# Performance work log

Hardware: AMD Instinct MI355X
Metric: run time of the kernel (lower is better)

Reference implementation:

```python
import jax, jax.numpy as jnp
import numpy as np

D_IN = 1024
D_OUT = 1024
N_HEADS = 16
HEAD_DIM = D_IN // N_HEADS      # 64
HEAD_DIM_V = D_OUT // N_HEADS   # 64


def setup_inputs() -> dict:
    key = jax.random.key(0)
    ks = jax.random.split(key, 7)
    s = 0.02
    x = jax.random.normal(ks[0], (4, 2048, D_IN), dtype=jnp.float32)
    Wq = jax.random.normal(ks[1], (D_IN, D_IN), dtype=jnp.float32) * s
    bq = jnp.zeros((D_IN,), dtype=jnp.float32)
    Wk = jax.random.normal(ks[2], (D_IN, D_IN), dtype=jnp.float32) * s
    bk = jnp.zeros((D_IN,), dtype=jnp.float32)
    Wv = jax.random.normal(ks[3], (D_IN, D_OUT), dtype=jnp.float32) * s
    bv = jnp.zeros((D_OUT,), dtype=jnp.float32)
    return {"x": x, "Wq": Wq, "bq": bq, "Wk": Wk, "bk": bk, "Wv": Wv, "bv": bv}


def reference(x, Wq, bq, Wk, bk, Wv, bv):
    B, S, _ = x.shape
    scale = jnp.sqrt(jnp.asarray(HEAD_DIM, dtype=jnp.float32))
    # projections -> [B, S, H, Dh] -> [B, H, S, Dh]
    q = (x @ Wq + bq).reshape(B, S, N_HEADS, HEAD_DIM).transpose(0, 2, 1, 3)
    k = (x @ Wk + bk).reshape(B, S, N_HEADS, HEAD_DIM).transpose(0, 2, 1, 3)
    v = (x @ Wv + bv).reshape(B, S, N_HEADS, HEAD_DIM_V).transpose(0, 2, 1, 3)
    # [B, H, S, S] attention scores (naive full materialization, as in source)
    scores = jnp.einsum("bhsd,bhtd->bhst", q, k) / scale
    weights = jax.nn.softmax(scores, axis=-1)
    out = jnp.einsum("bhst,bhtd->bhsd", weights, v)
    # [B, H, S, Dv] -> [B, S, H*Dv]  (out_projection NOT applied in source forward)
    return out.transpose(0, 2, 1, 3).reshape(B, S, N_HEADS * HEAD_DIM_V)
```

## Files before the change

### kernel.cpp

```cpp
#include <hip/hip_runtime.h>

#define B_  4
#define S_  2048
#define D_  1024
#define H_  16
#define DH_ 64
#define M_  (B_ * S_)

typedef __attribute__((ext_vector_type(8))) short short8;
typedef __attribute__((ext_vector_type(4))) float floatx4;

__device__ __forceinline__ float bf2f(unsigned short u) {
    union { unsigned int i; float f; } v; v.i = ((unsigned int)u) << 16; return v.f;
}
__device__ __forceinline__ unsigned short f2bf(float f) {
    union { float f; unsigned int i; } v; v.f = f;
    unsigned int r = v.i + 0x7fffu + ((v.i >> 16) & 1u);
    return (unsigned short)(r >> 16);
}
__device__ __forceinline__ unsigned int pk_trunc(float a, float b) {
#if __has_builtin(__builtin_amdgcn_perm)
    return __builtin_amdgcn_perm(__float_as_uint(b), __float_as_uint(a), 0x07060302u);
#else
    return (__float_as_uint(a) >> 16) | (__float_as_uint(b) & 0xffff0000u);
#endif
}

#if __has_builtin(__builtin_amdgcn_exp2f)
#define EXP2(x) __builtin_amdgcn_exp2f(x)
#else
#define EXP2(x) __expf(0.6931471805599453f * (x))
#endif

typedef const __attribute__((address_space(1))) unsigned int* gas_ptr;
typedef __attribute__((address_space(3))) unsigned int* las_ptr;
__device__ __forceinline__ void async_cp16(const void* g, void* l) {
    __builtin_amdgcn_global_load_lds((gas_ptr)g, (las_ptr)l, 16, 0, 0);
}

#define VMC4 asm volatile("s_waitcnt vmcnt(4)" ::: "memory")
#define VMC0 asm volatile("s_waitcnt vmcnt(0)" ::: "memory")

__global__ __launch_bounds__(256) void cast_x_kernel(
    const float* __restrict__ x, unsigned short* __restrict__ Ax)
{
    int i4 = blockIdx.x * 256 + threadIdx.x;
    float4 v = reinterpret_cast<const float4*>(x)[i4];
    ushort4 o;
    o.x = f2bf(v.x); o.y = f2bf(v.y); o.z = f2bf(v.z); o.w = f2bf(v.w);
    reinterpret_cast<ushort4*>(Ax)[i4] = o;
}

__global__ __launch_bounds__(256) void cast_w_T_kernel(
    const float* __restrict__ W0, const float* __restrict__ W1,
    const float* __restrict__ W2,
    unsigned short* __restrict__ T0, unsigned short* __restrict__ T1,
    unsigned short* __restrict__ T2)
{
    const float* W = blockIdx.z == 0 ? W0 : (blockIdx.z == 1 ? W1 : W2);
    unsigned short* Wt = blockIdx.z == 0 ? T0 : (blockIdx.z == 1 ? T1 : T2);

    __shared__ unsigned short T[64][72];
    const int t = threadIdx.x;
    const int k0 = blockIdx.x * 64, n0 = blockIdx.y * 64;

    #pragma unroll
    for (int p = 0; p < 4; ++p) {
        int kr = p * 16 + (t >> 4);
        int nc = (t & 15) * 4;
        float4 v = *reinterpret_cast<const float4*>(W + (size_t)(k0 + kr) * D_ + n0 + nc);
        T[nc + 0][kr] = f2bf(v.x);
        T[nc + 1][kr] = f2bf(v.y);
        T[nc + 2][kr] = f2bf(v.z);
        T[nc + 3][kr] = f2bf(v.w);
    }
    __syncthreads();

    const int nl = t >> 2, kc = (t & 3) * 16;
    size_t base = (size_t)(n0 + nl) * D_ + k0 + kc;
    *reinterpret_cast<short8*>(Wt + base)     = *reinterpret_cast<const short8*>(&T[nl][kc]);
    *reinterpret_cast<short8*>(Wt + base + 8) = *reinterpret_cast<const short8*>(&T[nl][kc + 8]);
}

__global__ __launch_bounds__(512) void gemm_qkv_mfma(
    const unsigned short* __restrict__ Ax,
    const unsigned short* __restrict__ Wtq,
    const unsigned short* __restrict__ Wtk,
    const unsigned short* __restrict__ Wtv,
    const float* __restrict__ bq, const float* __restrict__ bk,
    const float* __restrict__ bv,
    unsigned short* __restrict__ Q, unsigned short* __restrict__ K,
    unsigned short* __restrict__ Vtg)
{
    __shared__ unsigned short lds[65536];

    const int tid  = threadIdx.x;
    const int lane = tid & 63;
    const int w    = tid >> 6;
    const int wm   = w >> 2;
    const int wn   = w & 3;
    const int l15  = lane & 15, quad = lane >> 4;

    const int pl   = tid >> 3;
    const int sl   = tid & 7;
    const int xx   = sl ^ (pl & 7);
    const int sro  = pl * 2 + (xx >> 2);
    const int sc   = (xx & 3) * 8;
    const int ldst = tid * 8;

    const int fb = (l15 >> 1) * 64 + (((((l15 & 1) << 2) | quad)) ^ (l15 >> 1)) * 8;

    const int id  = blockIdx.x;
    const int wg  = (id & 7) * 48 + (id >> 3);
    const int nb  = wg >> 5;
    const int mb  = wg & 31;
    const int m0  = mb * 256;
    const int N0  = nb * 256;
    const int mat = N0 >> 10;
    const int n0m = N0 & 1023;

    const unsigned short* Wtb = mat == 0 ? Wtq : (mat == 1 ? Wtk : Wtv);
    const float* bias         = mat == 0 ? bq  : (mat == 1 ? bk  : bv);

    #define STG(G, rowbase, kcol, reg) do { \
        async_cp16((G) + (size_t)((rowbase) + sro) * 1024 + (kcol) + sc,       lds + (reg) + ldst); \
        async_cp16((G) + (size_t)((rowbase) + 128 + sro) * 1024 + (kcol) + sc, lds + (reg) + 4096 + ldst); \
    } while (0)

    floatx4 acc[8][4] = {};
    short8 bfr[4];

    STG(Ax,  m0,  0,  0);
    STG(Wtb, n0m, 0,  16384);
    STG(Ax,  m0,  32, 8192);
    STG(Wtb, n0m, 32, 24576);
    STG(Ax,  m0,  64, 32768);
    STG(Wtb, n0m, 64, 49152);
    VMC4;
    __builtin_amdgcn_s_barrier();

    #define PH(bufS, ksub, mh, STAGE_STMT, WAIT_STMT) do { \
        short8 af[4]; \
        _Pragma("unroll") \
        for (int i = 0; i < 4; ++i) \
            af[i] = *reinterpret_cast<const short8*>(lds + (bufS) + (ksub) * 8192 + wm * 4096 + ((mh) * 4 + i) * 512 + fb); \
        if ((mh) == 0) { \
            _Pragma("unroll") \
            for (int j = 0; j < 4; ++j) \
                bfr[j] = *reinterpret_cast<const short8*>(lds + (bufS) + 16384 + (ksub) * 8192 + wn * 2048 + j * 512 + fb); \
        } \
        STAGE_STMT; \
        __builtin_amdgcn_s_barrier(); \
        asm volatile("s_waitcnt lgkmcnt(0)" ::: "memory"); \
        __builtin_amdgcn_sched_barrier(0); \
        __builtin_amdgcn_s_setprio(1); \
        _Pragma("unroll") \
        for (int i = 0; i < 4; ++i) \
            _Pragma("unroll") \
            for (int j = 0; j < 4; ++j) \
                acc[(mh) * 4 + i][j] = __builtin_amdgcn_mfma_f32_16x16x32_bf16(af[i], bfr[j], acc[(mh) * 4 + i][j], 0, 0, 0); \
        __builtin_amdgcn_s_setprio(0); \
        WAIT_STMT; \
        __builtin_amdgcn_s_barrier(); \
    } while (0)

    #pragma unroll 1
    for (int it = 0; it < 8; ++it) {
        const int  t1 = 2 * it + 1;
        const bool nl = (it < 7);
        const int  kA = t1 * 64;
        const int  kB = kA + 64;
        const int  kC = kA + 128;
        PH(0,     0, 0, STG(Ax,  m0,  kA + 32, 40960), );
        PH(0,     0, 1, STG(Wtb, n0m, kA + 32, 57344), );
        PH(0,     1, 0, if (nl) STG(Ax,  m0,  kB, 0), );
        PH(0,     1, 1, if (nl) STG(Wtb, n0m, kB, 16384), { if (nl) VMC4; else VMC0; });
        PH(32768, 0, 0, if (nl) STG(Ax,  m0,  kB + 32, 8192), );
        PH(32768, 0, 1, if (nl) STG(Wtb, n0m, kB + 32, 24576), );
        PH(32768, 1, 0, if (nl) STG(Ax,  m0,  kC, 32768), );
        PH(32768, 1, 1, if (nl) STG(Wtb, n0m, kC, 49152), { if (nl) VMC4; });
    }

    float bb[4];
    #pragma unroll
    for (int j = 0; j < 4; ++j) bb[j] = bias[n0m + wn * 64 + j * 16 + l15];

    if (mat == 2) {
        const int bI    = m0 >> 11;
        const int sbase = (m0 & 2047) + wm * 128;
        #pragma unroll
        for (int mf = 0; mf < 8; ++mf) {
            int srow = sbase + mf * 16 + quad * 4;
            #pragma unroll
            for (int j = 0; j < 4; ++j) {
                int col = n0m + wn * 64 + j * 16 + l15;
                ushort4 o;
                o.x = f2bf(acc[mf][j][0] + bb[j]);
                o.y = f2bf(acc[mf][j][1] + bb[j]);
                o.z = f2bf(acc[mf][j][2] + bb[j]);
                o.w = f2bf(acc[mf][j][3] + bb[j]);
                *reinterpret_cast<ushort4*>(Vtg + (size_t)(bI * 1024 + col) * S_ + srow) = o;
            }
        }
    } else {
        unsigned short* C = (mat == 0) ? Q : K;
        const float scq = (mat == 0) ? 0.18033688011112042f : 1.0f;
        #pragma unroll
        for (int mf = 0; mf < 8; ++mf)
            #pragma unroll
            for (int r = 0; r < 4; ++r) {
                int row = m0 + wm * 128 + mf * 16 + quad * 4 + r;
                #pragma unroll
                for (int j = 0; j < 4; ++j)
                    C[(size_t)row * D_ + n0m + wn * 64 + j * 16 + l15] = f2bf((acc[mf][j][r] + bb[j]) * scq);
            }
    }
}

#define KT_   64
#define PITCH 72

__global__ __launch_bounds__(256, 4) void attn_mfma(
    const unsigned short* __restrict__ Qg,
    const unsigned short* __restrict__ Kg,
    const unsigned short* __restrict__ Vtg,
    float* __restrict__ out)
{
    __shared__ unsigned short Ks[KT_ * PITCH];
    __shared__ unsigned short Vt[DH_ * PITCH];

    const int tid  = threadIdx.x;
    const int wq   = tid >> 6;
    const int lane = tid & 63;
    const int l15  = lane & 15;
    const int quad = lane >> 4;

    const int id  = blockIdx.x;
    const int bh  = (id & 7) * 8 + ((id >> 3) & 7);
    const int qt  = id >> 6;
    const int b   = bh >> 4;
    const int colbase = (bh & 15) * DH_;
    const int rowQ0 = b * S_ + qt * 128;

    short8 qf[2][2];
    #pragma unroll
    for (int g = 0; g < 2; ++g) {
        int qrow = rowQ0 + wq * 32 + g * 16 + l15;
        qf[g][0] = *reinterpret_cast<const short8*>(Qg + (size_t)qrow * D_ + colbase + quad * 8);
        qf[g][1] = *reinterpret_cast<const short8*>(Qg + (size_t)qrow * D_ + colbase + 32 + quad * 8);
    }

    short8 vones;
    #pragma unroll
    for (int i = 0; i < 8; ++i) vones[i] = (short)0x3F80;

    floatx4 Oacc[2][4] = {};
    floatx4 Lacc[2] = {};

    const int srow = tid >> 3;
    const int sc8  = (tid & 7) * 8;
    const int vc  = sc8 >> 4;
    const int vqk = (sc8 >> 2) & 3;
    const int vk0 = ((vc & 1) << 2) + ((vc >> 1) << 5) + (vqk << 3);

    const unsigned short* Kbase = Kg + (size_t)(b * S_) * D_ + colbase;
    const unsigned short* Vbase = Vtg + (size_t)(bh * 64) * S_;

    short8 kpre[2], vpre[2];
    #pragma unroll
    for (int p = 0; p < 2; ++p) {
        kpre[p] = *reinterpret_cast<const short8*>(Kbase + (size_t)(p * 32 + srow) * D_ + sc8);
        vpre[p] = *reinterpret_cast<const short8*>(Vbase + (size_t)(p * 32 + srow) * S_ + sc8);
    }

    for (int kt = 0; kt < S_ / KT_; ++kt) {
        __syncthreads();
        #pragma unroll
        for (int p = 0; p < 2; ++p) {
            *reinterpret_cast<short8*>(&Ks[(p * 32 + srow) * PITCH + sc8]) = kpre[p];
            uint4 u = __builtin_bit_cast(uint4, vpre[p]);
            uint2 lo, hi;
            lo.x = u.x; lo.y = u.y; hi.x = u.z; hi.y = u.w;
            *reinterpret_cast<uint2*>(&Vt[(p * 32 + srow) * PITCH + vk0])     = lo;
            *reinterpret_cast<uint2*>(&Vt[(p * 32 + srow) * PITCH + vk0 + 8]) = hi;
        }
        if (kt + 1 < S_ / KT_) {
            int off = (kt + 1) * KT_;
            #pragma unroll
            for (int p = 0; p < 2; ++p) {
                kpre[p] = *reinterpret_cast<const short8*>(Kbase + (size_t)(off + p * 32 + srow) * D_ + sc8);
                vpre[p] = *reinterpret_cast<const short8*>(Vbase + (size_t)(p * 32 + srow) * S_ + off + sc8);
            }
        }
        __syncthreads();

        #pragma unroll
        for (int half = 0; half < 2; ++half) {
            floatx4 s_[2][2];
            #pragma unroll
            for (int ci = 0; ci < 2; ++ci) {
                int c = half * 2 + ci;
                short8 kf0 = *reinterpret_cast<const short8*>(&Ks[(c * 16 + l15) * PITCH + quad * 8]);
                short8 kf1 = *reinterpret_cast<const short8*>(&Ks[(c * 16 + l15) * PITCH + 32 + quad * 8]);
                #pragma unroll
                for (int g = 0; g < 2; ++g) {
                    floatx4 a = {0.f, 0.f, 0.f, 0.f};
                    a = __builtin_amdgcn_mfma_f32_16x16x32_bf16(kf0, qf[g][0], a, 0, 0, 0);
                    a = __builtin_amdgcn_mfma_f32_16x16x32_bf16(kf1, qf[g][1], a, 0, 0, 0);
                    s_[g][ci] = a;
                }
            }
            short8 pa[2];
            #pragma unroll
            for (int g = 0; g < 2; ++g) {
                float p00 = EXP2(s_[g][0][0]), p01 = EXP2(s_[g][0][1]);
                float p02 = EXP2(s_[g][0][2]), p03 = EXP2(s_[g][0][3]);
                float p10 = EXP2(s_[g][1][0]), p11 = EXP2(s_[g][1][1]);
                float p12 = EXP2(s_[g][1][2]), p13 = EXP2(s_[g][1][3]);
                uint4 pu;
                pu.x = pk_trunc(p00, p01);
                pu.y = pk_trunc(p02, p03);
                pu.z = pk_trunc(p10, p11);
                pu.w = pk_trunc(p12, p13);
                pa[g] = __builtin_bit_cast(short8, pu);
            }
            #pragma unroll
            for (int g = 0; g < 2; ++g)
                Lacc[g] = __builtin_amdgcn_mfma_f32_16x16x32_bf16(pa[g], vones, Lacc[g], 0, 0, 0);
            #pragma unroll
            for (int d = 0; d < 4; ++d) {
                short8 vf = *reinterpret_cast<const short8*>(
                    &Vt[(d * 16 + l15) * PITCH + half * 32 + quad * 8]);
                #pragma unroll
                for (int g = 0; g < 2; ++g)
                    Oacc[g][d] = __builtin_amdgcn_mfma_f32_16x16x32_bf16(pa[g], vf, Oacc[g][d], 0, 0, 0);
            }
        }
    }

    #pragma unroll
    for (int g = 0; g < 2; ++g) {
        int orow = rowQ0 + wq * 32 + g * 16 + quad * 4;
        #pragma unroll
        for (int r = 0; r < 4; ++r) {
            float inv = 1.f / Lacc[g][r];
            #pragma unroll
            for (int d = 0; d < 4; ++d)
                out[(size_t)(orow + r) * D_ + colbase + d * 16 + l15] = Oacc[g][d][r] * inv;
        }
    }
}

extern "C" void kernel_launch(void* const* d_in, const int* in_sizes, int n_in,
                              void* d_out, int out_size, void* d_ws, size_t ws_size,
                              hipStream_t stream) {
    const float* x  = (const float*)d_in[0];
    const float* Wq = (const float*)d_in[1];
    const float* bq = (const float*)d_in[2];
    const float* Wk = (const float*)d_in[3];
    const float* bk = (const float*)d_in[4];
    const float* Wv = (const float*)d_in[5];
    const float* bv = (const float*)d_in[6];
    float* out = (float*)d_out;

    unsigned short* Q   = (unsigned short*)d_ws;
    unsigned short* K   = Q + (size_t)M_ * D_;
    unsigned short* Vtg = K + (size_t)M_ * D_;
    unsigned short* Ax  = Vtg + (size_t)M_ * D_;
    unsigned short* Wtq = Ax + (size_t)M_ * D_;
    unsigned short* Wtk = Wtq + (size_t)D_ * D_;
    unsigned short* Wtv = Wtk + (size_t)D_ * D_;

    cast_x_kernel<<<M_ * D_ / 4 / 256, 256, 0, stream>>>(x, Ax);
    dim3 gw(16, 16, 3);
    cast_w_T_kernel<<<gw, 256, 0, stream>>>(Wq, Wk, Wv, Wtq, Wtk, Wtv);

    gemm_qkv_mfma<<<384, 512, 0, stream>>>(Ax, Wtq, Wtk, Wtv, bq, bk, bv, Q, K, Vtg);

    attn_mfma<<<1024, 256, 0, stream>>>(Q, K, Vtg, out);
}
```

Baseline: 243.6 us.

## Halve QKV GEMM M-tile to 128 and fuse cast kernels into one launch

The QKV projection GEMM moves from 256x256 tiles over 384 workgroups to 128x256 tiles over 768 workgroups. This cuts LDS use and accumulator registers so more blocks can fill the CUs, at the cost of reloading the weight tile for each extra M-block. The GEMM now addresses the contiguous Wt and Q/K buffers by offset instead of selecting per-matrix pointers. The x cast and the weight cast-transpose are merged into a single kernel launch, removing one launch boundary.

```diff
diff --git a/kernel.cpp b/kernel.cpp
--- a/kernel.cpp
+++ b/kernel.cpp
@@ -38,31 +38,34 @@
     __builtin_amdgcn_global_load_lds((gas_ptr)g, (las_ptr)l, 16, 0, 0);
 }
 
-#define VMC4 asm volatile("s_waitcnt vmcnt(4)" ::: "memory")
+#define VMC3 asm volatile("s_waitcnt vmcnt(3)" ::: "memory")
 #define VMC0 asm volatile("s_waitcnt vmcnt(0)" ::: "memory")
 
-__global__ __launch_bounds__(256) void cast_x_kernel(
-    const float* __restrict__ x, unsigned short* __restrict__ Ax)
-{
-    int i4 = blockIdx.x * 256 + threadIdx.x;
-    float4 v = reinterpret_cast<const float4*>(x)[i4];
-    ushort4 o;
-    o.x = f2bf(v.x); o.y = f2bf(v.y); o.z = f2bf(v.z); o.w = f2bf(v.w);
-    reinterpret_cast<ushort4*>(Ax)[i4] = o;
-}
-
-__global__ __launch_bounds__(256) void cast_w_T_kernel(
+__global__ __launch_bounds__(256) void cast_fused_kernel(
+    const float* __restrict__ x, unsigned short* __restrict__ Ax,
     const float* __restrict__ W0, const float* __restrict__ W1,
     const float* __restrict__ W2,
     unsigned short* __restrict__ T0, unsigned short* __restrict__ T1,
     unsigned short* __restrict__ T2)
 {
-    const float* W = blockIdx.z == 0 ? W0 : (blockIdx.z == 1 ? W1 : W2);
-    unsigned short* Wt = blockIdx.z == 0 ? T0 : (blockIdx.z == 1 ? T1 : T2);
+    const int bid = blockIdx.x;
+    const int t = threadIdx.x;
+    if (bid < 8192) {
+        int i4 = bid * 256 + t;
+        float4 v = reinterpret_cast<const float4*>(x)[i4];
+        ushort4 o;
+        o.x = f2bf(v.x); o.y = f2bf(v.y); o.z = f2bf(v.z); o.w = f2bf(v.w);
+        reinterpret_cast<ushort4*>(Ax)[i4] = o;
+        return;
+    }
+    const int idx = bid - 8192;
+    const int z   = idx >> 8;
+    const int rem = idx & 255;
+    const float* W = z == 0 ? W0 : (z == 1 ? W1 : W2);
+    unsigned short* Wt = z == 0 ? T0 : (z == 1 ? T1 : T2);
 
     __shared__ unsigned short T[64][72];
-    const int t = threadIdx.x;
-    const int k0 = blockIdx.x * 64, n0 = blockIdx.y * 64;
+    const int k0 = (rem & 15) * 64, n0 = (rem >> 4) * 64;
 
     #pragma unroll
     for (int p = 0; p < 4; ++p) {
@@ -84,15 +87,13 @@
 
 __global__ __launch_bounds__(512) void gemm_qkv_mfma(
     const unsigned short* __restrict__ Ax,
-    const unsigned short* __restrict__ Wtq,
-    const unsigned short* __restrict__ Wtk,
-    const unsigned short* __restrict__ Wtv,
+    const unsigned short* __restrict__ Wt,
     const float* __restrict__ bq, const float* __restrict__ bk,
     const float* __restrict__ bv,
-    unsigned short* __restrict__ Q, unsigned short* __restrict__ K,
+    unsigned short* __restrict__ Q,
     unsigned short* __restrict__ Vtg)
 {
-    __shared__ unsigned short lds[65536];
+    __shared__ unsigned short lds[49152];
 
     const int tid  = threadIdx.x;
     const int lane = tid & 63;
@@ -107,48 +108,41 @@
     const int sro  = pl * 2 + (xx >> 2);
     const int sc   = (xx & 3) * 8;
     const int ldst = tid * 8;
-
-    const int fb = (l15 >> 1) * 64 + (((((l15 & 1) << 2) | quad)) ^ (l15 >> 1)) * 8;
+    const int fb = (l15 >> 1) * 64 + ((((l15 & 1) << 2) | quad) ^ (l15 >> 1)) * 8;
 
     const int id  = blockIdx.x;
-    const int wg  = (id & 7) * 48 + (id >> 3);
-    const int nb  = wg >> 5;
-    const int mb  = wg & 31;
-    const int m0  = mb * 256;
-    const int N0  = nb * 256;
-    const int mat = N0 >> 10;
-    const int n0m = N0 & 1023;
-
-    const unsigned short* Wtb = mat == 0 ? Wtq : (mat == 1 ? Wtk : Wtv);
-    const float* bias         = mat == 0 ? bq  : (mat == 1 ? bk  : bv);
-
-    #define STG(G, rowbase, kcol, reg) do { \
-        async_cp16((G) + (size_t)((rowbase) + sro) * 1024 + (kcol) + sc,       lds + (reg) + ldst); \
-        async_cp16((G) + (size_t)((rowbase) + 128 + sro) * 1024 + (kcol) + sc, lds + (reg) + 4096 + ldst); \
+    const int g   = (id & 7) * 96 + (id >> 3);
+    const int nb  = g >> 6;
+    const int mb  = g & 63;
+    const int m0  = mb * 128;
+    const int n0g = nb * 256;
+    const int mat = nb >> 2;
+    const int n0m = (nb & 3) * 256;
+    const float* bias = mat == 0 ? bq : (mat == 1 ? bk : bv);
+
+    #define ASTG(kcol, reg) \
+        async_cp16(Ax + (size_t)(m0 + sro) * 1024 + (kcol) + sc, lds + (reg) + ldst)
+    #define BSTG(kcol, reg) do { \
+        async_cp16(Wt + (size_t)(n0g + sro) * 1024 + (kcol) + sc,       lds + (reg) + ldst); \
+        async_cp16(Wt + (size_t)(n0g + 128 + sro) * 1024 + (kcol) + sc, lds + (reg) + 4096 + ldst); \
     } while (0)
 
-    floatx4 acc[8][4] = {};
-    short8 bfr[4];
-
-    STG(Ax,  m0,  0,  0);
-    STG(Wtb, n0m, 0,  16384);
-    STG(Ax,  m0,  32, 8192);
-    STG(Wtb, n0m, 32, 24576);
-    STG(Ax,  m0,  64, 32768);
-    STG(Wtb, n0m, 64, 49152);
-    VMC4;
+    floatx4 acc[4][4] = {};
+
+    ASTG(0, 0);      BSTG(0, 8192);
+    ASTG(32, 4096);  BSTG(32, 16384);
+    ASTG(64, 24576); BSTG(64, 32768);
+    VMC3;
     __builtin_amdgcn_s_barrier();
 
-    #define PH(bufS, ksub, mh, STAGE_STMT, WAIT_STMT) do { \
-        short8 af[4]; \
+    #define PH(bufS, ksub, STAGE_STMT, WAIT_STMT) do { \
+        short8 af[4], bfr[4]; \
         _Pragma("unroll") \
         for (int i = 0; i < 4; ++i) \
-            af[i] = *reinterpret_cast<const short8*>(lds + (bufS) + (ksub) * 8192 + wm * 4096 + ((mh) * 4 + i) * 512 + fb); \
-        if ((mh) == 0) { \
-            _Pragma("unroll") \
-            for (int j = 0; j < 4; ++j) \
-                bfr[j] = *reinterpret_cast<const short8*>(lds + (bufS) + 16384 + (ksub) * 8192 + wn * 2048 + j * 512 + fb); \
-        } \
+            af[i] = *reinterpret_cast<const short8*>(lds + (bufS) + (ksub) * 4096 + wm * 2048 + i * 512 + fb); \
+        _Pragma("unroll") \
+        for (int j = 0; j < 4; ++j) \
+            bfr[j] = *reinterpret_cast<const short8*>(lds + (bufS) + 8192 + (ksub) * 8192 + wn * 2048 + j * 512 + fb); \
         STAGE_STMT; \
         __builtin_amdgcn_s_barrier(); \
         asm volatile("s_waitcnt lgkmcnt(0)" ::: "memory"); \
@@ -158,7 +152,7 @@
         for (int i = 0; i < 4; ++i) \
             _Pragma("unroll") \
             for (int j = 0; j < 4; ++j) \
-                acc[(mh) * 4 + i][j] = __builtin_amdgcn_mfma_f32_16x16x32_bf16(af[i], bfr[j], acc[(mh) * 4 + i][j], 0, 0, 0); \
+                acc[i][j] = __builtin_amdgcn_mfma_f32_16x16x32_bf16(af[i], bfr[j], acc[i][j], 0, 0, 0); \
         __builtin_amdgcn_s_setprio(0); \
         WAIT_STMT; \
         __builtin_amdgcn_s_barrier(); \
@@ -166,19 +160,14 @@
 
     #pragma unroll 1
     for (int it = 0; it < 8; ++it) {
-        const int  t1 = 2 * it + 1;
         const bool nl = (it < 7);
-        const int  kA = t1 * 64;
+        const int  kA = (2 * it + 1) * 64;
         const int  kB = kA + 64;
         const int  kC = kA + 128;
-        PH(0,     0, 0, STG(Ax,  m0,  kA + 32, 40960), );
-        PH(0,     0, 1, STG(Wtb, n0m, kA + 32, 57344), );
-        PH(0,     1, 0, if (nl) STG(Ax,  m0,  kB, 0), );
-        PH(0,     1, 1, if (nl) STG(Wtb, n0m, kB, 16384), { if (nl) VMC4; else VMC0; });
-        PH(32768, 0, 0, if (nl) STG(Ax,  m0,  kB + 32, 8192), );
-        PH(32768, 0, 1, if (nl) STG(Wtb, n0m, kB + 32, 24576), );
-        PH(32768, 1, 0, if (nl) STG(Ax,  m0,  kC, 32768), );
-        PH(32768, 1, 1, if (nl) STG(Wtb, n0m, kC, 49152), { if (nl) VMC4; });
+        PH(0,     0, { ASTG(kA + 32, 28672); BSTG(kA + 32, 40960); }, );
+        PH(0,     1, if (nl) { ASTG(kB, 0); BSTG(kB, 8192); }, { if (nl) VMC3; else VMC0; });
+        PH(24576, 0, if (nl) { ASTG(kB + 32, 4096); BSTG(kB + 32, 16384); }, );
+        PH(24576, 1, if (nl) { ASTG(kC, 24576); BSTG(kC, 32768); }, { if (nl) VMC3; });
     }
 
     float bb[4];
@@ -187,32 +176,31 @@
 
     if (mat == 2) {
         const int bI    = m0 >> 11;
-        const int sbase = (m0 & 2047) + wm * 128;
-        #pragma unroll
-        for (int mf = 0; mf < 8; ++mf) {
-            int srow = sbase + mf * 16 + quad * 4;
+        #pragma unroll
+        for (int i = 0; i < 4; ++i) {
+            int srow = (m0 & 2047) + wm * 64 + i * 16 + quad * 4;
             #pragma unroll
             for (int j = 0; j < 4; ++j) {
                 int col = n0m + wn * 64 + j * 16 + l15;
                 ushort4 o;
-                o.x = f2bf(acc[mf][j][0] + bb[j]);
-                o.y = f2bf(acc[mf][j][1] + bb[j]);
-                o.z = f2bf(acc[mf][j][2] + bb[j]);
-                o.w = f2bf(acc[mf][j][3] + bb[j]);
+                o.x = f2bf(acc[i][j][0] + bb[j]);
+                o.y = f2bf(acc[i][j][1] + bb[j]);
+                o.z = f2bf(acc[i][j][2] + bb[j]);
+                o.w = f2bf(acc[i][j][3] + bb[j]);
                 *reinterpret_cast<ushort4*>(Vtg + (size_t)(bI * 1024 + col) * S_ + srow) = o;
             }
         }
     } else {
-        unsigned short* C = (mat == 0) ? Q : K;
+        unsigned short* C = Q + (size_t)mat * M_ * D_;
         const float scq = (mat == 0) ? 0.18033688011112042f : 1.0f;
         #pragma unroll
-        for (int mf = 0; mf < 8; ++mf)
+        for (int i = 0; i < 4; ++i)
             #pragma unroll
             for (int r = 0; r < 4; ++r) {
-                int row = m0 + wm * 128 + mf * 16 + quad * 4 + r;
+                int row = m0 + wm * 64 + i * 16 + quad * 4 + r;
                 #pragma unroll
                 for (int j = 0; j < 4; ++j)
-                    C[(size_t)row * D_ + n0m + wn * 64 + j * 16 + l15] = f2bf((acc[mf][j][r] + bb[j]) * scq);
+                    C[(size_t)row * D_ + n0m + wn * 64 + j * 16 + l15] = f2bf((acc[i][j][r] + bb[j]) * scq);
             }
     }
 }
@@ -371,11 +359,9 @@
     unsigned short* Wtk = Wtq + (size_t)D_ * D_;
     unsigned short* Wtv = Wtk + (size_t)D_ * D_;
 
-    cast_x_kernel<<<M_ * D_ / 4 / 256, 256, 0, stream>>>(x, Ax);
-    dim3 gw(16, 16, 3);
-    cast_w_T_kernel<<<gw, 256, 0, stream>>>(Wq, Wk, Wv, Wtq, Wtk, Wtv);
-
-    gemm_qkv_mfma<<<384, 512, 0, stream>>>(Ax, Wtq, Wtk, Wtv, bq, bk, bv, Q, K, Vtg);
+    cast_fused_kernel<<<8192 + 768, 256, 0, stream>>>(x, Ax, Wq, Wk, Wv, Wtq, Wtk, Wtv);
+
+    gemm_qkv_mfma<<<768, 512, 0, stream>>>(Ax, Wtq, bq, bk, bv, Q, Vtg);
 
     attn_mfma<<<1024, 256, 0, stream>>>(Q, K, Vtg, out);
 }
```

Measured after the change: 228.8 us. 1.06x faster.
